# Kernel tuning notes

Hardware: AMD Instinct MI355X
Metric: run time of the kernel (lower is better)

## Reference

```python
import jax, jax.numpy as jnp
import numpy as np

HIDDEN = 2048
QUANTILES = 16
BATCH = 8192
HALF = HIDDEN // 2


def setup_inputs() -> dict:
    key = jax.random.key(0)
    kx, k1, kb1, k2 = jax.random.split(key, 4)
    x = jax.random.normal(kx, (BATCH, HIDDEN), dtype=jnp.float32)
    # Stacked per-head params: head q computes Linear(H->H/2) -> GELU -> Linear(H/2->1)
    # PyTorch Linear default init ~ U(-1/sqrt(fan_in), 1/sqrt(fan_in)); last layer kaiming-normal, bias 0.
    lim1 = 1.0 / np.sqrt(HIDDEN)
    W1 = jax.random.uniform(k1, (QUANTILES, HIDDEN, HALF), minval=-lim1, maxval=lim1, dtype=jnp.float32)
    b1 = jax.random.uniform(kb1, (QUANTILES, HALF), minval=-lim1, maxval=lim1, dtype=jnp.float32)
    # kaiming_normal fan_in, linear nonlinearity -> std = 1/sqrt(fan_in)
    W2 = jax.random.normal(k2, (QUANTILES, HALF), dtype=jnp.float32) / np.sqrt(HALF)
    b2 = jnp.zeros((QUANTILES,), dtype=jnp.float32)
    return {"x": x, "W1": W1, "b1": b1, "W2": W2, "b2": b2}


def reference(x, W1, b1, W2, b2):
    # Batched over all quantile heads: one grouped GEMM + fused GELU + grouped GEMV.
    # h: [batch, quantiles, half]
    h = jnp.einsum('bh,qhk->bqk', x, W1) + b1[None, :, :]
    h = jax.nn.gelu(h, approximate=False)  # torch nn.GELU() default = exact erf GELU
    # out: [batch, quantiles]
    out = jnp.einsum('bqk,qk->bq', h, W2) + b2[None, :]
    return out
```

## Files before the change

### kernel.cpp

```cpp
#include <hip/hip_runtime.h>

#define HIDDEN 2048
#define QUANT  16
#define BATCH  8192
#define HALFD  1024

typedef _Float16 half8  __attribute__((ext_vector_type(8)));
typedef _Float16 half4  __attribute__((ext_vector_type(4)));
typedef float    floatx4 __attribute__((ext_vector_type(4)));

__device__ __forceinline__ void load_lds16(const void* gptr, void* lptr) {
  __builtin_amdgcn_global_load_lds(
      (const __attribute__((address_space(1))) void*)gptr,
      (__attribute__((address_space(3))) void*)lptr, 16, 0, 0);
}

__device__ __forceinline__ float gelu_exact(float v) {
  const float z  = 0.7071067811865476f * v;
  const float az = fabsf(z);
  const float t  = __builtin_amdgcn_rcpf(1.0f + 0.3275911f * az);
  const float p  = t * (0.254829592f +
                   t * (-0.284496736f +
                   t * (1.421413741f +
                   t * (-1.453152027f +
                   t * 1.061405429f))));
  float er = 1.0f - p * __expf(-az * az);
  er = copysignf(er, z);
  return 0.5f * v * (1.0f + er);
}

__global__ __launch_bounds__(256) void convert_x_kernel(const float* __restrict__ x,
                                                        _Float16* __restrict__ xh) {
  const int i = (blockIdx.x * 256 + threadIdx.x) * 8;
  const float4 a = *(const float4*)(x + i);
  const float4 b = *(const float4*)(x + i + 4);
  half8 h;
  h[0] = (_Float16)a.x; h[1] = (_Float16)a.y; h[2] = (_Float16)a.z; h[3] = (_Float16)a.w;
  h[4] = (_Float16)b.x; h[5] = (_Float16)b.y; h[6] = (_Float16)b.z; h[7] = (_Float16)b.w;
  *(half8*)(xh + i) = h;
}

__global__ __launch_bounds__(256) void transpose_w1_kernel(const float* __restrict__ W1,
                                                           _Float16* __restrict__ W1T) {
  __shared__ float tile[32][33];
  const int q  = blockIdx.z;
  const int h0 = blockIdx.y * 32;
  const int n0 = blockIdx.x * 32;
  const float* src = W1 + (size_t)q * HIDDEN * HALFD;
  _Float16*    dst = W1T + (size_t)q * HALFD * HIDDEN;
  const int t = threadIdx.x;
  const int lx = t & 31, ly = t >> 5;
  #pragma unroll
  for (int j = 0; j < 4; ++j)
    tile[ly + 8 * j][lx] = src[(size_t)(h0 + ly + 8 * j) * HALFD + n0 + lx];
  __syncthreads();
  const int wy = t >> 3, wx = t & 7;
  half4 v;
  #pragma unroll
  for (int c = 0; c < 4; ++c) v[c] = (_Float16)tile[wx * 4 + c][wy];
  *(half4*)(dst + (size_t)(n0 + wy) * HIDDEN + h0 + wx * 4) = v;
}

__global__ __launch_bounds__(256) void init_out_kernel(float* __restrict__ out,
                                                       const float* __restrict__ b2) {
  const int i = blockIdx.x * 256 + threadIdx.x;
  out[i] = b2[i & (QUANT - 1)];
}

__global__ __launch_bounds__(256, 4) void qhead_gemm_kernel(
    const _Float16* __restrict__ A,
    const _Float16* __restrict__ BT,
    const float* __restrict__ b1,
    const float* __restrict__ W2,
    float* __restrict__ out) {
  __shared__ _Float16 As[64 * 64];
  __shared__ _Float16 Bs[128 * 64];

  const int tid  = threadIdx.x;
  const int lane = tid & 63;
  const int wave = tid >> 6;
  const int wm = wave >> 1, wn = wave & 1;
  const int lrow = lane & 15, quad = lane >> 4;

  const int m0 = blockIdx.y << 6;
  const int q  = blockIdx.x >> 3;
  const int n0 = (blockIdx.x & 7) << 7;

  const _Float16* Ablk = A + (size_t)m0 * HIDDEN;
  const _Float16* Bblk = BT + ((size_t)q * HALFD + n0) * HIDDEN;

  const int row_t = tid >> 3;
  const int gx = (((tid & 7) ^ (row_t & 7)) << 3);
  const _Float16* agp = Ablk + (size_t)row_t * HIDDEN + gx;
  const _Float16* bgp = Bblk + (size_t)row_t * HIDDEN + gx;
  _Float16* alp = &As[tid * 8];
  _Float16* blp = &Bs[tid * 8];

  int aoff[2], boff[4];
  #pragma unroll
  for (int f = 0; f < 2; ++f) aoff[f] = (wm * 32 + f * 16 + lrow) * 64;
  #pragma unroll
  for (int f = 0; f < 4; ++f) boff[f] = (wn * 64 + f * 16 + lrow) * 64;
  const int lxor = lrow & 7;

  floatx4 acc[2][4];
  #pragma unroll
  for (int mf = 0; mf < 2; ++mf)
    #pragma unroll
    for (int nf = 0; nf < 4; ++nf)
      acc[mf][nf] = (floatx4){0.f, 0.f, 0.f, 0.f};

  for (int kt = 0; kt < HIDDEN; kt += 64) {
    #pragma unroll
    for (int i = 0; i < 2; ++i)
      load_lds16(agp + (size_t)(i * 32) * HIDDEN + kt, alp + i * 2048);
    #pragma unroll
    for (int i = 0; i < 4; ++i)
      load_lds16(bgp + (size_t)(i * 32) * HIDDEN + kt, blp + i * 2048);
    __syncthreads();

    #pragma unroll
    for (int ks = 0; ks < 2; ++ks) {
      const int kxo = ((((ks << 2) | quad) ^ lxor) << 3);
      half8 af[2], bf[4];
      #pragma unroll
      for (int mf = 0; mf < 2; ++mf) af[mf] = *(const half8*)&As[aoff[mf] + kxo];
      #pragma unroll
      for (int nf = 0; nf < 4; ++nf) bf[nf] = *(const half8*)&Bs[boff[nf] + kxo];
      #pragma unroll
      for (int mf = 0; mf < 2; ++mf)
        #pragma unroll
        for (int nf = 0; nf < 4; ++nf)
          acc[mf][nf] = __builtin_amdgcn_mfma_f32_16x16x32_f16(af[mf], bf[nf], acc[mf][nf], 0, 0, 0);
    }
    __syncthreads();
  }

  const int nbase = n0 + wn * 64;
  float rowsum[2][4];
  #pragma unroll
  for (int mf = 0; mf < 2; ++mf)
    #pragma unroll
    for (int i = 0; i < 4; ++i) rowsum[mf][i] = 0.f;

  #pragma unroll
  for (int nf = 0; nf < 4; ++nf) {
    const int ncol = nbase + nf * 16 + lrow;
    const float b1v = b1[q * HALFD + ncol];
    const float w2v = W2[q * HALFD + ncol];
    #pragma unroll
    for (int mf = 0; mf < 2; ++mf) {
      #pragma unroll
      for (int i = 0; i < 4; ++i) {
        rowsum[mf][i] += gelu_exact(acc[mf][nf][i] + b1v) * w2v;
      }
    }
  }
  #pragma unroll
  for (int mf = 0; mf < 2; ++mf) {
    #pragma unroll
    for (int i = 0; i < 4; ++i) {
      float t = rowsum[mf][i];
      t += __shfl_xor(t, 1, 64);
      t += __shfl_xor(t, 2, 64);
      t += __shfl_xor(t, 4, 64);
      t += __shfl_xor(t, 8, 64);
      rowsum[mf][i] = t;
    }
  }
  if (lrow == 0) {
    #pragma unroll
    for (int mf = 0; mf < 2; ++mf) {
      const int mrow = m0 + wm * 32 + mf * 16 + quad * 4;
      #pragma unroll
      for (int i = 0; i < 4; ++i)
        atomicAdd(&out[(size_t)(mrow + i) * QUANT + q], rowsum[mf][i]);
    }
  }
}

extern "C" void kernel_launch(void* const* d_in, const int* in_sizes, int n_in,
                              void* d_out, int out_size, void* d_ws, size_t ws_size,
                              hipStream_t stream) {
  const float* x  = (const float*)d_in[0];
  const float* W1 = (const float*)d_in[1];
  const float* b1 = (const float*)d_in[2];
  const float* W2 = (const float*)d_in[3];
  const float* b2 = (const float*)d_in[4];
  float* out = (float*)d_out;

  _Float16* xh  = (_Float16*)d_ws;
  _Float16* w1t = (_Float16*)((char*)d_ws +
                  (size_t)BATCH * HIDDEN * sizeof(_Float16));

  convert_x_kernel<<<BATCH * HIDDEN / (256 * 8), 256, 0, stream>>>(x, xh);
  transpose_w1_kernel<<<dim3(HALFD / 32, HIDDEN / 32, QUANT), 256, 0, stream>>>(W1, w1t);
  init_out_kernel<<<BATCH * QUANT / 256, 256, 0, stream>>>(out, b2);
  qhead_gemm_kernel<<<dim3(128, 128), 256, 0, stream>>>(xh, w1t, b1, W2, out);
}
```

Before: 1.064 ms.

## Enlarge GEMM tile to 128x128 with 32x32 MFMA and vectorize W1 transpose

The grouped GEMM block tile grows from 64x128 to 128x128, and the inner product switches from 16x16x32 to 32x32x16 MFMA with 64x64 per-wave tiles. This raises arithmetic intensity and reuse of the LDS data, and halves the grid. The epilogue reduction is adapted to the 32x32 accumulator layout, adding an extra shuffle step and handling more rows per lane. The W1 transpose now uses float4 loads and half8 stores over 64-row tiles to cut memory transactions. In exchange, accumulator register pressure rises and fewer blocks are launched.

Measured after the change: 904.6 us. 1.18x faster.

```diff
diff --git a/kernel.cpp b/kernel.cpp
--- a/kernel.cpp
+++ b/kernel.cpp
@@ -6,8 +6,7 @@
 #define HALFD  1024
 
 typedef _Float16 half8  __attribute__((ext_vector_type(8)));
-typedef _Float16 half4  __attribute__((ext_vector_type(4)));
-typedef float    floatx4 __attribute__((ext_vector_type(4)));
+typedef float    floatx16 __attribute__((ext_vector_type(16)));
 
 __device__ __forceinline__ void load_lds16(const void* gptr, void* lptr) {
   __builtin_amdgcn_global_load_lds(
@@ -42,23 +41,30 @@
 
 __global__ __launch_bounds__(256) void transpose_w1_kernel(const float* __restrict__ W1,
                                                            _Float16* __restrict__ W1T) {
-  __shared__ float tile[32][33];
+  __shared__ float tile[64][33];
   const int q  = blockIdx.z;
-  const int h0 = blockIdx.y * 32;
+  const int h0 = blockIdx.y * 64;
   const int n0 = blockIdx.x * 32;
   const float* src = W1 + (size_t)q * HIDDEN * HALFD;
   _Float16*    dst = W1T + (size_t)q * HALFD * HIDDEN;
-  const int t = threadIdx.x;
-  const int lx = t & 31, ly = t >> 5;
-  #pragma unroll
-  for (int j = 0; j < 4; ++j)
-    tile[ly + 8 * j][lx] = src[(size_t)(h0 + ly + 8 * j) * HALFD + n0 + lx];
+  const int t  = threadIdx.x;
+  const int lr = t >> 3;
+  const int lc = (t & 7) * 4;
+  #pragma unroll
+  for (int j = 0; j < 2; ++j) {
+    const float4 v = *(const float4*)(src + (size_t)(h0 + lr + 32 * j) * HALFD + n0 + lc);
+    tile[lr + 32 * j][lc + 0] = v.x;
+    tile[lr + 32 * j][lc + 1] = v.y;
+    tile[lr + 32 * j][lc + 2] = v.z;
+    tile[lr + 32 * j][lc + 3] = v.w;
+  }
   __syncthreads();
-  const int wy = t >> 3, wx = t & 7;
-  half4 v;
-  #pragma unroll
-  for (int c = 0; c < 4; ++c) v[c] = (_Float16)tile[wx * 4 + c][wy];
-  *(half4*)(dst + (size_t)(n0 + wy) * HIDDEN + h0 + wx * 4) = v;
+  const int sn = t >> 3;
+  const int sh = (t & 7) * 8;
+  half8 v;
+  #pragma unroll
+  for (int c = 0; c < 8; ++c) v[c] = (_Float16)tile[sh + c][sn];
+  *(half8*)(dst + (size_t)(n0 + sn) * HIDDEN + h0 + sh) = v;
 }
 
 __global__ __launch_bounds__(256) void init_out_kernel(float* __restrict__ out,
@@ -73,16 +79,16 @@
     const float* __restrict__ b1,
     const float* __restrict__ W2,
     float* __restrict__ out) {
-  __shared__ _Float16 As[64 * 64];
+  __shared__ _Float16 As[128 * 64];
   __shared__ _Float16 Bs[128 * 64];
 
   const int tid  = threadIdx.x;
   const int lane = tid & 63;
   const int wave = tid >> 6;
   const int wm = wave >> 1, wn = wave & 1;
-  const int lrow = lane & 15, quad = lane >> 4;
-
-  const int m0 = blockIdx.y << 6;
+  const int r31 = lane & 31, l5 = lane >> 5, lx = lane & 7;
+
+  const int m0 = blockIdx.y << 7;
   const int q  = blockIdx.x >> 3;
   const int n0 = (blockIdx.x & 7) << 7;
 
@@ -96,23 +102,24 @@
   _Float16* alp = &As[tid * 8];
   _Float16* blp = &Bs[tid * 8];
 
-  int aoff[2], boff[4];
-  #pragma unroll
-  for (int f = 0; f < 2; ++f) aoff[f] = (wm * 32 + f * 16 + lrow) * 64;
-  #pragma unroll
-  for (int f = 0; f < 4; ++f) boff[f] = (wn * 64 + f * 16 + lrow) * 64;
-  const int lxor = lrow & 7;
-
-  floatx4 acc[2][4];
+  int aoff[2], boff[2];
+  #pragma unroll
+  for (int f = 0; f < 2; ++f) {
+    aoff[f] = (wm * 64 + f * 32 + r31) * 64;
+    boff[f] = (wn * 64 + f * 32 + r31) * 64;
+  }
+
+  floatx16 acc[2][2];
   #pragma unroll
   for (int mf = 0; mf < 2; ++mf)
     #pragma unroll
-    for (int nf = 0; nf < 4; ++nf)
-      acc[mf][nf] = (floatx4){0.f, 0.f, 0.f, 0.f};
+    for (int nf = 0; nf < 2; ++nf)
+      #pragma unroll
+      for (int i = 0; i < 16; ++i) acc[mf][nf][i] = 0.f;
 
   for (int kt = 0; kt < HIDDEN; kt += 64) {
     #pragma unroll
-    for (int i = 0; i < 2; ++i)
+    for (int i = 0; i < 4; ++i)
       load_lds16(agp + (size_t)(i * 32) * HIDDEN + kt, alp + i * 2048);
     #pragma unroll
     for (int i = 0; i < 4; ++i)
@@ -120,61 +127,62 @@
     __syncthreads();
 
     #pragma unroll
-    for (int ks = 0; ks < 2; ++ks) {
-      const int kxo = ((((ks << 2) | quad) ^ lxor) << 3);
-      half8 af[2], bf[4];
-      #pragma unroll
-      for (int mf = 0; mf < 2; ++mf) af[mf] = *(const half8*)&As[aoff[mf] + kxo];
-      #pragma unroll
-      for (int nf = 0; nf < 4; ++nf) bf[nf] = *(const half8*)&Bs[boff[nf] + kxo];
+    for (int ks = 0; ks < 4; ++ks) {
+      const int p = (((ks << 1) | l5) ^ lx) << 3;
+      half8 af[2], bf[2];
+      #pragma unroll
+      for (int mf = 0; mf < 2; ++mf) af[mf] = *(const half8*)&As[aoff[mf] + p];
+      #pragma unroll
+      for (int nf = 0; nf < 2; ++nf) bf[nf] = *(const half8*)&Bs[boff[nf] + p];
       #pragma unroll
       for (int mf = 0; mf < 2; ++mf)
         #pragma unroll
-        for (int nf = 0; nf < 4; ++nf)
-          acc[mf][nf] = __builtin_amdgcn_mfma_f32_16x16x32_f16(af[mf], bf[nf], acc[mf][nf], 0, 0, 0);
+        for (int nf = 0; nf < 2; ++nf)
+          acc[mf][nf] = __builtin_amdgcn_mfma_f32_32x32x16_f16(af[mf], bf[nf], acc[mf][nf], 0, 0, 0);
     }
     __syncthreads();
   }
 
   const int nbase = n0 + wn * 64;
-  float rowsum[2][4];
+  float rowsum[2][16];
   #pragma unroll
   for (int mf = 0; mf < 2; ++mf)
     #pragma unroll
-    for (int i = 0; i < 4; ++i) rowsum[mf][i] = 0.f;
-
-  #pragma unroll
-  for (int nf = 0; nf < 4; ++nf) {
-    const int ncol = nbase + nf * 16 + lrow;
+    for (int r = 0; r < 16; ++r) rowsum[mf][r] = 0.f;
+
+  #pragma unroll
+  for (int nf = 0; nf < 2; ++nf) {
+    const int ncol = nbase + nf * 32 + r31;
     const float b1v = b1[q * HALFD + ncol];
     const float w2v = W2[q * HALFD + ncol];
     #pragma unroll
-    for (int mf = 0; mf < 2; ++mf) {
-      #pragma unroll
-      for (int i = 0; i < 4; ++i) {
-        rowsum[mf][i] += gelu_exact(acc[mf][nf][i] + b1v) * w2v;
-      }
-    }
+    for (int mf = 0; mf < 2; ++mf)
+      #pragma unroll
+      for (int r = 0; r < 16; ++r)
+        rowsum[mf][r] += gelu_exact(acc[mf][nf][r] + b1v) * w2v;
   }
   #pragma unroll
   for (int mf = 0; mf < 2; ++mf) {
     #pragma unroll
-    for (int i = 0; i < 4; ++i) {
-      float t = rowsum[mf][i];
+    for (int r = 0; r < 16; ++r) {
+      float t = rowsum[mf][r];
       t += __shfl_xor(t, 1, 64);
       t += __shfl_xor(t, 2, 64);
       t += __shfl_xor(t, 4, 64);
       t += __shfl_xor(t, 8, 64);
-      rowsum[mf][i] = t;
+      t += __shfl_xor(t, 16, 64);
+      rowsum[mf][r] = t;
     }
   }
-  if (lrow == 0) {
+  if (r31 == 0) {
     #pragma unroll
     for (int mf = 0; mf < 2; ++mf) {
-      const int mrow = m0 + wm * 32 + mf * 16 + quad * 4;
-      #pragma unroll
-      for (int i = 0; i < 4; ++i)
-        atomicAdd(&out[(size_t)(mrow + i) * QUANT + q], rowsum[mf][i]);
+      const int mbase = m0 + wm * 64 + mf * 32 + 4 * l5;
+      #pragma unroll
+      for (int r = 0; r < 16; ++r) {
+        const int mrow = mbase + (r & 3) + 8 * (r >> 2);
+        atomicAdd(&out[(size_t)mrow * QUANT + q], rowsum[mf][r]);
+      }
     }
   }
 }
@@ -194,7 +202,7 @@
                   (size_t)BATCH * HIDDEN * sizeof(_Float16));
 
   convert_x_kernel<<<BATCH * HIDDEN / (256 * 8), 256, 0, stream>>>(x, xh);
-  transpose_w1_kernel<<<dim3(HALFD / 32, HIDDEN / 32, QUANT), 256, 0, stream>>>(W1, w1t);
+  transpose_w1_kernel<<<dim3(HALFD / 32, HIDDEN / 64, QUANT), 256, 0, stream>>>(W1, w1t);
   init_out_kernel<<<BATCH * QUANT / 256, 256, 0, stream>>>(out, b2);
-  qhead_gemm_kernel<<<dim3(128, 128), 256, 0, stream>>>(xh, w1t, b1, W2, out);
-}
+  qhead_gemm_kernel<<<dim3(128, 64), 256, 0, stream>>>(xh, w1t, b1, W2, out);
+}
```
